# Optimization experiments

Measured on AMD Instinct MI355X. Metric: run time of the kernel, lower is better.

The kernel has to match this reference:

```python
import jax, jax.numpy as jnp
import numpy as np

N, E = 50000, 800000
C, H, EC = 64, 3, 32  # node_channels, heads, edge_channels
NEG_SLOPE = 0.2


def _kaiming(key, shape, fan_in):
    bound = np.sqrt(6.0 / fan_in)  # kaiming_uniform_ default (a=sqrt(5)-ish approx; gain sqrt(2) variant)
    return jax.random.uniform(key, shape, jnp.float32, -bound, bound)


def setup_inputs() -> dict:
    key = jax.random.key(0)
    ks = jax.random.split(key, 8)
    x = jax.random.normal(ks[0], (N, C), jnp.float32)
    edge_index = jax.random.randint(ks[1], (2, E), 0, N, jnp.int64)
    edge_attr = jax.random.normal(ks[2], (E, EC), jnp.float32)
    weight_node = _kaiming(ks[3], (C, H * C), C)
    weight_edge = _kaiming(ks[4], (EC, H * C), EC)
    weight_triplet_att = _kaiming(ks[5], (1, H, 3 * C), 3 * C)
    weight_scale = _kaiming(ks[6], (H * C, C), H * C)
    bias = jnp.zeros((C,), jnp.float32)
    return {"x": x, "edge_index": edge_index, "edge_attr": edge_attr,
            "weight_node": weight_node, "weight_edge": weight_edge,
            "weight_triplet_att": weight_triplet_att,
            "weight_scale": weight_scale, "bias": bias}


def reference(x, edge_index, edge_attr, weight_node, weight_edge,
              weight_triplet_att, weight_scale, bias):
    src = edge_index[0]  # j (source)
    dst = edge_index[1]  # i (target), PyG default flow source_to_target

    xp = x @ weight_node                     # [N, H*C]
    ep = edge_attr @ weight_edge             # [E, H*C]

    x_j = xp[src].reshape(E, H, C)
    x_i = xp[dst].reshape(E, H, C)
    e_ij = ep.reshape(E, H, C)

    # attention weight split along concat order [x_i, e_ij, x_j]
    w = weight_triplet_att.reshape(H, 3, C)
    alpha = (jnp.einsum('ehc,hc->eh', x_i, w[:, 0])
             + jnp.einsum('ehc,hc->eh', e_ij, w[:, 1])
             + jnp.einsum('ehc,hc->eh', x_j, w[:, 2]))   # [E, H]
    alpha = jnp.where(alpha >= 0, alpha, NEG_SLOPE * alpha)  # leaky_relu

    # segment softmax over destination nodes (PyG softmax semantics)
    seg_max = jax.ops.segment_max(alpha, dst, num_segments=N)    # [N, H]
    alpha = jnp.exp(alpha - seg_max[dst])
    seg_sum = jax.ops.segment_sum(alpha, dst, num_segments=N)    # [N, H]
    alpha = alpha / (seg_sum[dst] + 1e-16)

    msg = alpha[:, :, None] * e_ij * x_j                         # [E, H, C]
    aggr = jax.ops.segment_sum(msg.reshape(E, H * C), dst, num_segments=N)  # [N, H*C]

    return aggr @ weight_scale + bias                            # [N, C]
```

## Files before the change

### kernel.cpp

```cpp
#include <hip/hip_runtime.h>

#define CC    64
#define HH    3
#define ECC   32
#define HCdim 192
#define NEG_SLOPE 0.2f
#define ASHIFT 12.0f
#define LOG2E  1.44269504f

typedef float v2f __attribute__((ext_vector_type(2)));
typedef _Float16 h2 __attribute__((ext_vector_type(2)));
typedef _Float16 h8 __attribute__((ext_vector_type(8)));

#if defined(__has_builtin)
#  if __has_builtin(__builtin_amdgcn_fdot2)
#    define USE_FDOT2 1
#  endif
#endif
#ifndef USE_FDOT2
#  define USE_FDOT2 0
#endif

__global__ void tm_k0(const float* __restrict__ We, const float* __restrict__ wt,
                      float* __restrict__ u) {
    int t = threadIdx.x;
    if (t >= HH * ECC) return;
    int h = t >> 5, k = t & 31;
    float s = 0.f;
    #pragma unroll
    for (int c = 0; c < CC; ++c)
        s = fmaf(We[k * HCdim + h * CC + c], wt[h * HCdim + CC + c], s);
    u[t] = s;
}

#define K1_ROWS 64
__global__ __launch_bounds__(192) void tm_k1(const float* __restrict__ x,
        const float* __restrict__ Wn, const float* __restrict__ wt,
        const int* __restrict__ ei, int* __restrict__ deg,
        _Float16* __restrict__ xp16, float* __restrict__ sA, int N, int E) {
    __shared__ float wl[CC * HCdim];
    __shared__ float xl[K1_ROWS * CC];
    const int t = threadIdx.x;
    for (int i = blockIdx.x * 192 + t; i < E; i += gridDim.x * 192)
        atomicAdd(&deg[ei[E + i]], 1);
    const int h = t >> 6, c = t & 63;
    {
        float4* wl4 = (float4*)wl;
        const float4* Wn4 = (const float4*)Wn;
        for (int i = t; i < CC * HCdim / 4; i += 192) wl4[i] = Wn4[i];
    }
    const int base = blockIdx.x * K1_ROWS;
    const int rows = min(K1_ROWS, N - base);
    {
        float4* xl4 = (float4*)xl;
        const float4* x4 = (const float4*)(x + (size_t)base * CC);
        for (int i = t; i < rows * CC / 4; i += 192) xl4[i] = x4[i];
    }
    const float w0c = wt[h * HCdim + c];
    const float w2c = wt[h * HCdim + 2 * CC + c];
    __syncthreads();
    for (int rt = 0; rt < rows; rt += 4) {
        float acc0 = 0.f, acc1 = 0.f, acc2 = 0.f, acc3 = 0.f;
        #pragma unroll 4
        for (int k = 0; k < CC; k += 4) {
            const float w0  = wl[(k + 0) * HCdim + t];
            const float w1  = wl[(k + 1) * HCdim + t];
            const float w2_ = wl[(k + 2) * HCdim + t];
            const float w3  = wl[(k + 3) * HCdim + t];
            const float4 xa = *(const float4*)&xl[(rt + 0) * CC + k];
            const float4 xb = *(const float4*)&xl[(rt + 1) * CC + k];
            const float4 xc = *(const float4*)&xl[(rt + 2) * CC + k];
            const float4 xd = *(const float4*)&xl[(rt + 3) * CC + k];
            acc0 = fmaf(xa.x, w0, fmaf(xa.y, w1, fmaf(xa.z, w2_, fmaf(xa.w, w3, acc0))));
            acc1 = fmaf(xb.x, w0, fmaf(xb.y, w1, fmaf(xb.z, w2_, fmaf(xb.w, w3, acc1))));
            acc2 = fmaf(xc.x, w0, fmaf(xc.y, w1, fmaf(xc.z, w2_, fmaf(xc.w, w3, acc2))));
            acc3 = fmaf(xd.x, w0, fmaf(xd.y, w1, fmaf(xd.z, w2_, fmaf(xd.w, w3, acc3))));
        }
        #pragma unroll
        for (int r = 0; r < 4; ++r) {
            const float v = (r == 0) ? acc0 : (r == 1) ? acc1 : (r == 2) ? acc2 : acc3;
            const int n = base + rt + r;
            xp16[(size_t)n * HCdim + t] = (_Float16)v;
            float a0 = v * w0c, a2 = v * w2c;
            #pragma unroll
            for (int o = 32; o; o >>= 1) {
                a0 += __shfl_xor(a0, o);
                a2 += __shfl_xor(a2, o);
            }
            if (c == 0) {
                sA[n * 8 + h]     = a0;
                sA[n * 8 + 4 + h] = a2;
            }
        }
    }
}

__global__ __launch_bounds__(256) void tm_scanA(const int* __restrict__ deg,
        int* __restrict__ bsum, int N) {
    __shared__ int sd[256];
    int t = threadIdx.x, n = blockIdx.x * 256 + t;
    sd[t] = (n < N) ? deg[n] : 0;
    __syncthreads();
    for (int o = 128; o; o >>= 1) {
        if (t < o) sd[t] += sd[t + o];
        __syncthreads();
    }
    if (!t) bsum[blockIdx.x] = sd[0];
}

__global__ __launch_bounds__(256) void tm_scanB(const int* __restrict__ bsum,
        int* __restrict__ boff, int nb) {
    __shared__ int sd[256];
    int t = threadIdx.x;
    int v = (t < nb) ? bsum[t] : 0;
    sd[t] = v;
    __syncthreads();
    for (int o = 1; o < 256; o <<= 1) {
        int x = (t >= o) ? sd[t - o] : 0;
        __syncthreads();
        sd[t] += x;
        __syncthreads();
    }
    if (t < nb) boff[t] = sd[t] - v;
}

__global__ __launch_bounds__(256) void tm_scanC(const int* __restrict__ deg,
        const int* __restrict__ boff, int* __restrict__ off,
        int* __restrict__ cursor, int N) {
    __shared__ int sd[256];
    int t = threadIdx.x, n = blockIdx.x * 256 + t;
    int v = (n < N) ? deg[n] : 0;
    sd[t] = v;
    __syncthreads();
    for (int o = 1; o < 256; o <<= 1) {
        int x = (t >= o) ? sd[t - o] : 0;
        __syncthreads();
        sd[t] += x;
        __syncthreads();
    }
    if (n < N) {
        int ex = boff[blockIdx.x] + sd[t] - v;
        off[n] = ex;
        cursor[n] = ex;
        if (n == N - 1) off[N] = ex + v;
    }
}

__global__ __launch_bounds__(256) void tm_alpha(const int* __restrict__ ei,
        const float* __restrict__ ea, const float* __restrict__ u,
        const float* __restrict__ sA, int* __restrict__ cursor,
        float4* __restrict__ alphaE, int2* __restrict__ perm,
        _Float16* __restrict__ ea16, int E) {
    __shared__ float ul[HH * ECC];
    const int t = threadIdx.x;
    if (t < HH * ECC) ul[t] = u[t];
    __syncthreads();
    const int e = blockIdx.x * 256 + t;
    if (e >= E) return;
    const int src = ei[e];
    const int dst = ei[E + e];
    float av[ECC];
    const float4* p4 = (const float4*)(ea + (size_t)e * ECC);
    #pragma unroll
    for (int q = 0; q < 8; ++q) {
        float4 v = p4[q];
        av[4*q] = v.x; av[4*q+1] = v.y; av[4*q+2] = v.z; av[4*q+3] = v.w;
    }
#if USE_FDOT2
    {
        h8* dst16 = (h8*)(ea16 + (size_t)e * ECC);
        #pragma unroll
        for (int b = 0; b < 4; ++b) {
            h8 o16;
            #pragma unroll
            for (int j = 0; j < 8; ++j) o16[j] = (_Float16)av[b * 8 + j];
            dst16[b] = o16;
        }
    }
#else
    (void)ea16;
#endif
    float d0 = 0.f, d1 = 0.f, d2 = 0.f;
    #pragma unroll
    for (int k = 0; k < ECC; ++k) {
        d0 = fmaf(av[k], ul[k], d0);
        d1 = fmaf(av[k], ul[ECC + k], d1);
        d2 = fmaf(av[k], ul[2 * ECC + k], d2);
    }
    const float4 s0 = *(const float4*)(sA + (size_t)dst * 8);
    const float4 s2 = *(const float4*)(sA + (size_t)src * 8 + 4);
    float a0 = s0.x + d0 + s2.x;
    float a1 = s0.y + d1 + s2.y;
    float a2 = s0.z + d2 + s2.z;
    a0 = (a0 >= 0.f) ? a0 : NEG_SLOPE * a0;
    a1 = (a1 >= 0.f) ? a1 : NEG_SLOPE * a1;
    a2 = (a2 >= 0.f) ? a2 : NEG_SLOPE * a2;
    alphaE[e] = make_float4(exp2f((a0 - ASHIFT) * LOG2E),
                            exp2f((a1 - ASHIFT) * LOG2E),
                            exp2f((a2 - ASHIFT) * LOG2E), 0.f);
    const int pos = atomicAdd(&cursor[dst], 1);
    perm[pos] = make_int2(src * (HCdim * 2), e * (ECC * 4));
}

__global__ __launch_bounds__(192) void tm_agg(const int2* __restrict__ perm,
        const int* __restrict__ off, const float* __restrict__ ea,
        const float* __restrict__ We, const float* __restrict__ alphaE,
        const _Float16* __restrict__ xp16, const _Float16* __restrict__ ea16,
        float* __restrict__ aggrN, int N) {
    const int t = threadIdx.x;
    const int h = t >> 6, lane = t & 63;
    const char* __restrict__ xp_b = (const char*)xp16;
    const char* __restrict__ al_b = (const char*)alphaE;
#if USE_FDOT2
    const char* __restrict__ e16_b = (const char*)ea16;
    h2 wc[16];
    #pragma unroll
    for (int k2 = 0; k2 < 16; ++k2) {
        h2 w;
        w[0] = (_Float16)We[(2 * k2)     * HCdim + h * CC + lane];
        w[1] = (_Float16)We[(2 * k2 + 1) * HCdim + h * CC + lane];
        wc[k2] = w;
    }
#else
    const char* __restrict__ ea_b = (const char*)ea;
    (void)ea16;
    v2f wcol2[16];
    #pragma unroll
    for (int k2 = 0; k2 < 16; ++k2) {
        wcol2[k2].x = We[(2 * k2)     * HCdim + h * CC + lane];
        wcol2[k2].y = We[(2 * k2 + 1) * HCdim + h * CC + lane];
    }
#endif
    const int xoff = h * (CC * 2) + lane * 2;
    const int aoff = h * 4;
    for (int n = blockIdx.x; n < N; n += gridDim.x) {
        const int start = off[n], end = off[n + 1];
        float s = 0.f, acc = 0.f;
        int pos = start;
        int4 pp = (pos + 2 <= end) ? *(const int4*)&perm[pos]
                                   : make_int4(0, 0, 0, 0);
        for (; pos + 2 <= end; ) {
            const int4 cur = pp;
            pos += 2;
            if (pos + 2 <= end) pp = *(const int4*)&perm[pos];
            const int so0 = __builtin_amdgcn_readfirstlane(cur.x);
            const int eo0 = __builtin_amdgcn_readfirstlane(cur.y);
            const int so1 = __builtin_amdgcn_readfirstlane(cur.z);
            const int eo1 = __builtin_amdgcn_readfirstlane(cur.w);
            const float p0 = *(const float*)(al_b + (eo0 >> 3) + aoff);
            const float p1 = *(const float*)(al_b + (eo1 >> 3) + aoff);
            const float xj0 = (float)*(const _Float16*)(xp_b + so0 + xoff);
            const float xj1 = (float)*(const _Float16*)(xp_b + so1 + xoff);
            float ep0, ep1;
#if USE_FDOT2
            const uint4 a0 = *(const uint4*)(e16_b + (eo0 >> 1));
            const uint4 a1 = *(const uint4*)(e16_b + (eo0 >> 1) + 16);
            const uint4 b0 = *(const uint4*)(e16_b + (eo1 >> 1));
            const uint4 b1 = *(const uint4*)(e16_b + (eo1 >> 1) + 16);
            float d0 = 0.f, d1 = 0.f;
            d0 = __builtin_amdgcn_fdot2(__builtin_bit_cast(h2, a0.x), wc[0], d0, false);
            d0 = __builtin_amdgcn_fdot2(__builtin_bit_cast(h2, a0.y), wc[1], d0, false);
            d0 = __builtin_amdgcn_fdot2(__builtin_bit_cast(h2, a0.z), wc[2], d0, false);
            d0 = __builtin_amdgcn_fdot2(__builtin_bit_cast(h2, a0.w), wc[3], d0, false);
            d0 = __builtin_amdgcn_fdot2(__builtin_bit_cast(h2, a1.x), wc[4], d0, false);
            d0 = __builtin_amdgcn_fdot2(__builtin_bit_cast(h2, a1.y), wc[5], d0, false);
            d0 = __builtin_amdgcn_fdot2(__builtin_bit_cast(h2, a1.z), wc[6], d0, false);
            d0 = __builtin_amdgcn_fdot2(__builtin_bit_cast(h2, a1.w), wc[7], d0, false);
            const uint4 a2 = *(const uint4*)(e16_b + (eo0 >> 1) + 32);
            const uint4 a3 = *(const uint4*)(e16_b + (eo0 >> 1) + 48);
            d0 = __builtin_amdgcn_fdot2(__builtin_bit_cast(h2, a2.x), wc[8],  d0, false);
            d0 = __builtin_amdgcn_fdot2(__builtin_bit_cast(h2, a2.y), wc[9],  d0, false);
            d0 = __builtin_amdgcn_fdot2(__builtin_bit_cast(h2, a2.z), wc[10], d0, false);
            d0 = __builtin_amdgcn_fdot2(__builtin_bit_cast(h2, a2.w), wc[11], d0, false);
            d0 = __builtin_amdgcn_fdot2(__builtin_bit_cast(h2, a3.x), wc[12], d0, false);
            d0 = __builtin_amdgcn_fdot2(__builtin_bit_cast(h2, a3.y), wc[13], d0, false);
            d0 = __builtin_amdgcn_fdot2(__builtin_bit_cast(h2, a3.z), wc[14], d0, false);
            d0 = __builtin_amdgcn_fdot2(__builtin_bit_cast(h2, a3.w), wc[15], d0, false);
            const uint4 b2 = *(const uint4*)(e16_b + (eo1 >> 1) + 32);
            const uint4 b3 = *(const uint4*)(e16_b + (eo1 >> 1) + 48);
            d1 = __builtin_amdgcn_fdot2(__builtin_bit_cast(h2, b0.x), wc[0],  d1, false);
            d1 = __builtin_amdgcn_fdot2(__builtin_bit_cast(h2, b0.y), wc[1],  d1, false);
            d1 = __builtin_amdgcn_fdot2(__builtin_bit_cast(h2, b0.z), wc[2],  d1, false);
            d1 = __builtin_amdgcn_fdot2(__builtin_bit_cast(h2, b0.w), wc[3],  d1, false);
            d1 = __builtin_amdgcn_fdot2(__builtin_bit_cast(h2, b1.x), wc[4],  d1, false);
            d1 = __builtin_amdgcn_fdot2(__builtin_bit_cast(h2, b1.y), wc[5],  d1, false);
            d1 = __builtin_amdgcn_fdot2(__builtin_bit_cast(h2, b1.z), wc[6],  d1, false);
            d1 = __builtin_amdgcn_fdot2(__builtin_bit_cast(h2, b1.w), wc[7],  d1, false);
            d1 = __builtin_amdgcn_fdot2(__builtin_bit_cast(h2, b2.x), wc[8],  d1, false);
            d1 = __builtin_amdgcn_fdot2(__builtin_bit_cast(h2, b2.y), wc[9],  d1, false);
            d1 = __builtin_amdgcn_fdot2(__builtin_bit_cast(h2, b2.z), wc[10], d1, false);
            d1 = __builtin_amdgcn_fdot2(__builtin_bit_cast(h2, b2.w), wc[11], d1, false);
            d1 = __builtin_amdgcn_fdot2(__builtin_bit_cast(h2, b3.x), wc[12], d1, false);
            d1 = __builtin_amdgcn_fdot2(__builtin_bit_cast(h2, b3.y), wc[13], d1, false);
            d1 = __builtin_amdgcn_fdot2(__builtin_bit_cast(h2, b3.z), wc[14], d1, false);
            d1 = __builtin_amdgcn_fdot2(__builtin_bit_cast(h2, b3.w), wc[15], d1, false);
            ep0 = d0; ep1 = d1;
#else
            const float4* q0 = (const float4*)(ea_b + eo0);
            const float4* q1 = (const float4*)(ea_b + eo1);
            v2f d0 = {0.f, 0.f}, d1 = {0.f, 0.f};
            #pragma unroll
            for (int q = 0; q < 8; ++q) {
                const float4 v0 = q0[q];
                const float4 v1 = q1[q];
                const v2f wlo = wcol2[2 * q], whi = wcol2[2 * q + 1];
                d0 = (v2f){v0.x, v0.y} * wlo + d0;
                d0 = (v2f){v0.z, v0.w} * whi + d0;
                d1 = (v2f){v1.x, v1.y} * wlo + d1;
                d1 = (v2f){v1.z, v1.w} * whi + d1;
            }
            ep0 = d0.x + d0.y; ep1 = d1.x + d1.y;
#endif
            s += p0 + p1;
            acc = fmaf(p0 * ep0, xj0, acc);
            acc = fmaf(p1 * ep1, xj1, acc);
        }
        if (pos < end) {
            const int2 pe = perm[pos];
            const int so = __builtin_amdgcn_readfirstlane(pe.x);
            const int eo = __builtin_amdgcn_readfirstlane(pe.y);
            const float p = *(const float*)(al_b + (eo >> 3) + aoff);
            const float xj = (float)*(const _Float16*)(xp_b + so + xoff);
            float ep;
#if USE_FDOT2
            const uint4 a0 = *(const uint4*)(e16_b + (eo >> 1));
            const uint4 a1 = *(const uint4*)(e16_b + (eo >> 1) + 16);
            const uint4 a2 = *(const uint4*)(e16_b + (eo >> 1) + 32);
            const uint4 a3 = *(const uint4*)(e16_b + (eo >> 1) + 48);
            float d = 0.f;
            d = __builtin_amdgcn_fdot2(__builtin_bit_cast(h2, a0.x), wc[0],  d, false);
            d = __builtin_amdgcn_fdot2(__builtin_bit_cast(h2, a0.y), wc[1],  d, false);
            d = __builtin_amdgcn_fdot2(__builtin_bit_cast(h2, a0.z), wc[2],  d, false);
            d = __builtin_amdgcn_fdot2(__builtin_bit_cast(h2, a0.w), wc[3],  d, false);
            d = __builtin_amdgcn_fdot2(__builtin_bit_cast(h2, a1.x), wc[4],  d, false);
            d = __builtin_amdgcn_fdot2(__builtin_bit_cast(h2, a1.y), wc[5],  d, false);
            d = __builtin_amdgcn_fdot2(__builtin_bit_cast(h2, a1.z), wc[6],  d, false);
            d = __builtin_amdgcn_fdot2(__builtin_bit_cast(h2, a1.w), wc[7],  d, false);
            d = __builtin_amdgcn_fdot2(__builtin_bit_cast(h2, a2.x), wc[8],  d, false);
            d = __builtin_amdgcn_fdot2(__builtin_bit_cast(h2, a2.y), wc[9],  d, false);
            d = __builtin_amdgcn_fdot2(__builtin_bit_cast(h2, a2.z), wc[10], d, false);
            d = __builtin_amdgcn_fdot2(__builtin_bit_cast(h2, a2.w), wc[11], d, false);
            d = __builtin_amdgcn_fdot2(__builtin_bit_cast(h2, a3.x), wc[12], d, false);
            d = __builtin_amdgcn_fdot2(__builtin_bit_cast(h2, a3.y), wc[13], d, false);
            d = __builtin_amdgcn_fdot2(__builtin_bit_cast(h2, a3.z), wc[14], d, false);
            d = __builtin_amdgcn_fdot2(__builtin_bit_cast(h2, a3.w), wc[15], d, false);
            ep = d;
#else
            const float4* q4 = (const float4*)(ea_b + eo);
            v2f d = {0.f, 0.f};
            #pragma unroll
            for (int q = 0; q < 8; ++q) {
                const float4 v = q4[q];
                d = (v2f){v.x, v.y} * wcol2[2 * q]     + d;
                d = (v2f){v.z, v.w} * wcol2[2 * q + 1] + d;
            }
            ep = d.x + d.y;
#endif
            s += p;
            acc = fmaf(p * ep, xj, acc);
        }
        aggrN[(size_t)n * HCdim + h * CC + lane] = acc / (s + 1e-16f);
    }
}

#define K5_ROWS 16
__global__ __launch_bounds__(256) void tm_k5(const float* __restrict__ aggrN,
        const float* __restrict__ Ws, const float* __restrict__ bias,
        float* __restrict__ out, int N) {
    __shared__ float wsl[HCdim * CC];
    __shared__ float al[K5_ROWS * HCdim];
    const int t = threadIdx.x;
    const int part = t >> 6, c = t & 63;
    {
        float4* w4 = (float4*)wsl;
        const float4* Ws4 = (const float4*)Ws;
        for (int i = t; i < HCdim * CC / 4; i += 256) w4[i] = Ws4[i];
    }
    const float b = bias[c];
    for (int base = blockIdx.x * K5_ROWS; base < N; base += gridDim.x * K5_ROWS) {
        const int rows = min(K5_ROWS, N - base);
        __syncthreads();
        {
            float4* al4 = (float4*)al;
            const float4* a4 = (const float4*)(aggrN + (size_t)base * HCdim);
            for (int i = t; i < rows * HCdim / 4; i += 256) al4[i] = a4[i];
        }
        __syncthreads();
        const int r0 = part * 4;
        if (r0 >= rows) continue;
        float acc0 = b, acc1 = b, acc2 = b, acc3 = b;
        #pragma unroll 4
        for (int k = 0; k < HCdim; k += 4) {
            const float w0  = wsl[(k + 0) * CC + c];
            const float w1  = wsl[(k + 1) * CC + c];
            const float w2_ = wsl[(k + 2) * CC + c];
            const float w3  = wsl[(k + 3) * CC + c];
            const float4 xa = *(const float4*)&al[(r0 + 0) * HCdim + k];
            const float4 xb = *(const float4*)&al[(r0 + 1) * HCdim + k];
            const float4 xc = *(const float4*)&al[(r0 + 2) * HCdim + k];
            const float4 xd = *(const float4*)&al[(r0 + 3) * HCdim + k];
            acc0 = fmaf(xa.x, w0, fmaf(xa.y, w1, fmaf(xa.z, w2_, fmaf(xa.w, w3, acc0))));
            acc1 = fmaf(xb.x, w0, fmaf(xb.y, w1, fmaf(xb.z, w2_, fmaf(xb.w, w3, acc1))));
            acc2 = fmaf(xc.x, w0, fmaf(xc.y, w1, fmaf(xc.z, w2_, fmaf(xc.w, w3, acc2))));
            acc3 = fmaf(xd.x, w0, fmaf(xd.y, w1, fmaf(xd.z, w2_, fmaf(xd.w, w3, acc3))));
        }
        if (r0 + 0 < rows) out[(size_t)(base + r0 + 0) * CC + c] = acc0;
        if (r0 + 1 < rows) out[(size_t)(base + r0 + 1) * CC + c] = acc1;
        if (r0 + 2 < rows) out[(size_t)(base + r0 + 2) * CC + c] = acc2;
        if (r0 + 3 < rows) out[(size_t)(base + r0 + 3) * CC + c] = acc3;
    }
}

extern "C" void kernel_launch(void* const* d_in, const int* in_sizes, int n_in,
                              void* d_out, int out_size, void* d_ws, size_t ws_size,
                              hipStream_t stream) {
    const float* x    = (const float*)d_in[0];
    const int*   ei   = (const int*)d_in[1];
    const float* ea   = (const float*)d_in[2];
    const float* Wn   = (const float*)d_in[3];
    const float* We   = (const float*)d_in[4];
    const float* wt   = (const float*)d_in[5];
    const float* Ws   = (const float*)d_in[6];
    const float* bias = (const float*)d_in[7];
    float* out = (float*)d_out;
    const int N = in_sizes[0] / CC;
    const int E = in_sizes[1] / 2;
    const int nb = (N + 255) / 256;

    float* ws = (float*)d_ws;
    size_t o = 0;
    _Float16* xp16 = (_Float16*)(ws + o); o += (size_t)N * HCdim / 2;
    float* sA = ws + o;                  o += (size_t)N * 8;
    float* u  = ws + o;                  o += 128;
    float4* alphaE = (float4*)(ws + o);  o += (size_t)E * 4;
    int2*  perm = (int2*)(ws + o);       o += (size_t)E * 2 + 32;
    _Float16* ea16 = (_Float16*)(ws + o); o += (size_t)E * ECC / 2;
    int* deg    = (int*)(ws + o);        o += N;
    int* off    = (int*)(ws + o);        o += N + 1;
    int* cursor = (int*)(ws + o);        o += N;
    int* bsum   = (int*)(ws + o);        o += 256;
    int* boff   = (int*)(ws + o);        o += 256;
    o += (4 - (o & 3)) & 3;
    float* aggrN = ws + o;               o += (size_t)N * HCdim;
    (void)ws_size; (void)n_in; (void)out_size;

    (void)hipMemsetAsync(deg, 0, (size_t)N * sizeof(int), stream);

    tm_k0<<<1, 96, 0, stream>>>(We, wt, u);
    tm_k1<<<(N + K1_ROWS - 1) / K1_ROWS, 192, 0, stream>>>(x, Wn, wt, ei, deg,
                                                           xp16, sA, N, E);
    tm_scanA<<<nb, 256, 0, stream>>>(deg, bsum, N);
    tm_scanB<<<1, 256, 0, stream>>>(bsum, boff, nb);
    tm_scanC<<<nb, 256, 0, stream>>>(deg, boff, off, cursor, N);
    tm_alpha<<<(E + 255) / 256, 256, 0, stream>>>(ei, ea, u, sA, cursor,
                                                  alphaE, perm, ea16, E);
    tm_agg<<<(N + 7) / 8, 192, 0, stream>>>(perm, off, ea, We,
                                            (const float*)alphaE, xp16, ea16,
                                            aggrN, N);
    tm_k5<<<512, 256, 0, stream>>>(aggrN, Ws, bias, out, N);
}
```

Measured before the change: 387.8 us.

## Fuse output projection into aggregation kernel, dropping aggrN buffer and k5 launch

The final aggr @ weight_scale + bias projection moves into the per-node aggregation kernel. Each thread holds a 64-entry slice of Ws in registers (fp16 pairs when fdot2 is available) and computes a partial dot product from the normalized aggregate staged in shared memory. The three head partials are reduced through shared memory with two block barriers per node. This removes the N×192 float intermediate round trip and one kernel launch, but adds register pressure, per-node syncs, and fp16 rounding of the projection inputs.

```diff
diff --git a/kernel.cpp b/kernel.cpp
--- a/kernel.cpp
+++ b/kernel.cpp
@@ -204,9 +204,12 @@
 
 __global__ __launch_bounds__(192) void tm_agg(const int2* __restrict__ perm,
         const int* __restrict__ off, const float* __restrict__ ea,
-        const float* __restrict__ We, const float* __restrict__ alphaE,
+        const float* __restrict__ We, const float* __restrict__ Ws,
+        const float* __restrict__ bias, const float* __restrict__ alphaE,
         const _Float16* __restrict__ xp16, const _Float16* __restrict__ ea16,
-        float* __restrict__ aggrN, int N) {
+        float* __restrict__ out, int N) {
+    __shared__ __align__(16) float alv[HCdim];
+    __shared__ float pp[HCdim];
     const int t = threadIdx.x;
     const int h = t >> 6, lane = t & 63;
     const char* __restrict__ xp_b = (const char*)xp16;
@@ -221,6 +224,14 @@
         w[1] = (_Float16)We[(2 * k2 + 1) * HCdim + h * CC + lane];
         wc[k2] = w;
     }
+    h2 wsr[32];
+    #pragma unroll
+    for (int j = 0; j < 32; ++j) {
+        h2 w;
+        w[0] = (_Float16)Ws[(h * CC + 2 * j)     * CC + lane];
+        w[1] = (_Float16)Ws[(h * CC + 2 * j + 1) * CC + lane];
+        wsr[j] = w;
+    }
 #else
     const char* __restrict__ ea_b = (const char*)ea;
     (void)ea16;
@@ -230,19 +241,24 @@
         wcol2[k2].x = We[(2 * k2)     * HCdim + h * CC + lane];
         wcol2[k2].y = We[(2 * k2 + 1) * HCdim + h * CC + lane];
     }
-#endif
+    float wsr32[64];
+    #pragma unroll
+    for (int j = 0; j < 64; ++j)
+        wsr32[j] = Ws[(h * CC + j) * CC + lane];
+#endif
+    const float b = bias[lane];
     const int xoff = h * (CC * 2) + lane * 2;
     const int aoff = h * 4;
     for (int n = blockIdx.x; n < N; n += gridDim.x) {
         const int start = off[n], end = off[n + 1];
         float s = 0.f, acc = 0.f;
         int pos = start;
-        int4 pp = (pos + 2 <= end) ? *(const int4*)&perm[pos]
-                                   : make_int4(0, 0, 0, 0);
+        int4 pp4 = (pos + 2 <= end) ? *(const int4*)&perm[pos]
+                                    : make_int4(0, 0, 0, 0);
         for (; pos + 2 <= end; ) {
-            const int4 cur = pp;
+            const int4 cur = pp4;
             pos += 2;
-            if (pos + 2 <= end) pp = *(const int4*)&perm[pos];
+            if (pos + 2 <= end) pp4 = *(const int4*)&perm[pos];
             const int so0 = __builtin_amdgcn_readfirstlane(cur.x);
             const int eo0 = __builtin_amdgcn_readfirstlane(cur.y);
             const int so1 = __builtin_amdgcn_readfirstlane(cur.z);
@@ -359,55 +375,37 @@
             s += p;
             acc = fmaf(p * ep, xj, acc);
         }
-        aggrN[(size_t)n * HCdim + h * CC + lane] = acc / (s + 1e-16f);
-    }
-}
-
-#define K5_ROWS 16
-__global__ __launch_bounds__(256) void tm_k5(const float* __restrict__ aggrN,
-        const float* __restrict__ Ws, const float* __restrict__ bias,
-        float* __restrict__ out, int N) {
-    __shared__ float wsl[HCdim * CC];
-    __shared__ float al[K5_ROWS * HCdim];
-    const int t = threadIdx.x;
-    const int part = t >> 6, c = t & 63;
-    {
-        float4* w4 = (float4*)wsl;
-        const float4* Ws4 = (const float4*)Ws;
-        for (int i = t; i < HCdim * CC / 4; i += 256) w4[i] = Ws4[i];
-    }
-    const float b = bias[c];
-    for (int base = blockIdx.x * K5_ROWS; base < N; base += gridDim.x * K5_ROWS) {
-        const int rows = min(K5_ROWS, N - base);
-        __syncthreads();
+        alv[h * CC + lane] = acc / (s + 1e-16f);
+        __syncthreads();
+        float part = 0.f;
         {
-            float4* al4 = (float4*)al;
-            const float4* a4 = (const float4*)(aggrN + (size_t)base * HCdim);
-            for (int i = t; i < rows * HCdim / 4; i += 256) al4[i] = a4[i];
-        }
-        __syncthreads();
-        const int r0 = part * 4;
-        if (r0 >= rows) continue;
-        float acc0 = b, acc1 = b, acc2 = b, acc3 = b;
-        #pragma unroll 4
-        for (int k = 0; k < HCdim; k += 4) {
-            const float w0  = wsl[(k + 0) * CC + c];
-            const float w1  = wsl[(k + 1) * CC + c];
-            const float w2_ = wsl[(k + 2) * CC + c];
-            const float w3  = wsl[(k + 3) * CC + c];
-            const float4 xa = *(const float4*)&al[(r0 + 0) * HCdim + k];
-            const float4 xb = *(const float4*)&al[(r0 + 1) * HCdim + k];
-            const float4 xc = *(const float4*)&al[(r0 + 2) * HCdim + k];
-            const float4 xd = *(const float4*)&al[(r0 + 3) * HCdim + k];
-            acc0 = fmaf(xa.x, w0, fmaf(xa.y, w1, fmaf(xa.z, w2_, fmaf(xa.w, w3, acc0))));
-            acc1 = fmaf(xb.x, w0, fmaf(xb.y, w1, fmaf(xb.z, w2_, fmaf(xb.w, w3, acc1))));
-            acc2 = fmaf(xc.x, w0, fmaf(xc.y, w1, fmaf(xc.z, w2_, fmaf(xc.w, w3, acc2))));
-            acc3 = fmaf(xd.x, w0, fmaf(xd.y, w1, fmaf(xd.z, w2_, fmaf(xd.w, w3, acc3))));
-        }
-        if (r0 + 0 < rows) out[(size_t)(base + r0 + 0) * CC + c] = acc0;
-        if (r0 + 1 < rows) out[(size_t)(base + r0 + 1) * CC + c] = acc1;
-        if (r0 + 2 < rows) out[(size_t)(base + r0 + 2) * CC + c] = acc2;
-        if (r0 + 3 < rows) out[(size_t)(base + r0 + 3) * CC + c] = acc3;
+            const float4* a4 = (const float4*)&alv[h * CC];
+#if USE_FDOT2
+            #pragma unroll
+            for (int j4 = 0; j4 < 16; ++j4) {
+                const float4 av4 = a4[j4];
+                h2 lo, hi;
+                lo[0] = (_Float16)av4.x; lo[1] = (_Float16)av4.y;
+                hi[0] = (_Float16)av4.z; hi[1] = (_Float16)av4.w;
+                part = __builtin_amdgcn_fdot2(lo, wsr[2 * j4],     part, false);
+                part = __builtin_amdgcn_fdot2(hi, wsr[2 * j4 + 1], part, false);
+            }
+#else
+            #pragma unroll
+            for (int j4 = 0; j4 < 16; ++j4) {
+                const float4 av4 = a4[j4];
+                part = fmaf(av4.x, wsr32[4 * j4 + 0],
+                       fmaf(av4.y, wsr32[4 * j4 + 1],
+                       fmaf(av4.z, wsr32[4 * j4 + 2],
+                       fmaf(av4.w, wsr32[4 * j4 + 3], part))));
+            }
+#endif
+        }
+        pp[h * CC + lane] = part;
+        __syncthreads();
+        if (h == 0)
+            out[(size_t)n * CC + lane] =
+                pp[lane] + pp[CC + lane] + pp[2 * CC + lane] + b;
     }
 }
 
@@ -440,8 +438,6 @@
     int* cursor = (int*)(ws + o);        o += N;
     int* bsum   = (int*)(ws + o);        o += 256;
     int* boff   = (int*)(ws + o);        o += 256;
-    o += (4 - (o & 3)) & 3;
-    float* aggrN = ws + o;               o += (size_t)N * HCdim;
     (void)ws_size; (void)n_in; (void)out_size;
 
     (void)hipMemsetAsync(deg, 0, (size_t)N * sizeof(int), stream);
@@ -454,8 +450,7 @@
     tm_scanC<<<nb, 256, 0, stream>>>(deg, boff, off, cursor, N);
     tm_alpha<<<(E + 255) / 256, 256, 0, stream>>>(ei, ea, u, sA, cursor,
                                                   alphaE, perm, ea16, E);
-    tm_agg<<<(N + 7) / 8, 192, 0, stream>>>(perm, off, ea, We,
+    tm_agg<<<(N + 7) / 8, 192, 0, stream>>>(perm, off, ea, We, Ws, bias,
                                             (const float*)alphaE, xp16, ea16,
-                                            aggrN, N);
-    tm_k5<<<512, 256, 0, stream>>>(aggrN, Ws, bias, out, N);
-}
+                                            out, N);
+}
```

New measurement: 415.2 us. 7.0% more time.
